# Optimization experiments

Hardware: AMD Instinct MI355X
Metric: run time of the kernel (lower is better)

## Reference

```python
import jax, jax.numpy as jnp
import numpy as np

NUM_HEADS = 16


def setup_inputs() -> dict:
    key = jax.random.key(0)
    ks = jax.random.split(key, 11)
    S, E, F = 4096, 2048, 8192
    s = lambda k, shape, fan_in: jax.random.normal(k, shape, jnp.float32) / np.sqrt(fan_in)
    return {
        "emb": jax.random.normal(ks[0], (S, E), jnp.float32),
        "Wq": s(ks[1], (E, E), E), "bq": jnp.zeros((E,), jnp.float32),
        "Wk": s(ks[2], (E, E), E), "bk": jnp.zeros((E,), jnp.float32),
        "Wv": s(ks[3], (E, E), E), "bv": jnp.zeros((E,), jnp.float32),
        "W1": s(ks[4], (E, F), E), "b1": jnp.zeros((F,), jnp.float32),
        "W2": s(ks[5], (F, E), F), "b2": jnp.zeros((E,), jnp.float32),
    }


def reference(emb, Wq, bq, Wk, bk, Wv, bv, W1, b1, W2, b2):
    S, E = emb.shape
    H = NUM_HEADS
    D = E // H
    # project and split heads -> [H, S, D]
    q = (emb @ Wq + bq).reshape(S, H, D).transpose(1, 0, 2)
    k = (emb @ Wk + bk).reshape(S, H, D).transpose(1, 0, 2)
    v = (emb @ Wv + bv).reshape(S, H, D).transpose(1, 0, 2)
    scale = jnp.asarray(D, emb.dtype) ** 0.5
    scores = jnp.einsum("hsd,htd->hst", q, k) / scale  # [H, S, S]
    # causal mask: additive -1e9 strictly above the diagonal (matches torch.triu(..., 1)*-1e9)
    mask = jnp.triu(jnp.full((S, S), -1e9, dtype=scores.dtype), k=1)
    probs = jax.nn.softmax(scores + mask, axis=-1)
    attn = jnp.einsum("hst,htd->hsd", probs, v)  # [H, S, D]
    attn = attn.transpose(1, 0, 2).reshape(S, E)  # concat heads -> [S, E]
    hidden = jnp.maximum(attn @ W1 + b1, 0.0)
    return hidden @ W2 + b2
```

## Files before the change

### kernel.cpp

```cpp
#include <hip/hip_runtime.h>

typedef __attribute__((ext_vector_type(8))) short bf16x8;
typedef __attribute__((ext_vector_type(4))) float f32x4;
typedef __attribute__((ext_vector_type(8))) unsigned short u16x8;

static constexpr int S = 4096;
static constexpr int E = 2048;
static constexpr int F = 8192;
static constexpr int NH = 16;
static constexpr int DH = 128;

__device__ __forceinline__ unsigned short f2bf(float f) {
  unsigned u = __builtin_bit_cast(unsigned, f);
  u += 0x7FFFu + ((u >> 16) & 1u);
  return (unsigned short)(u >> 16);
}

__device__ __forceinline__ void async16(const unsigned short* g, unsigned short* l) {
  __builtin_amdgcn_global_load_lds(
      (const __attribute__((address_space(1))) unsigned int*)g,
      (__attribute__((address_space(3))) unsigned int*)l, 16, 0, 0);
}

__global__ __launch_bounds__(256) void cvt_bf16_kernel(const float* __restrict__ src,
                                                       unsigned short* __restrict__ dst) {
  int i = (blockIdx.x * 256 + threadIdx.x) * 4;
  float4 v = *(const float4*)(src + i);
  ushort4 o;
  o.x = f2bf(v.x); o.y = f2bf(v.y); o.z = f2bf(v.z); o.w = f2bf(v.w);
  *(ushort4*)(dst + i) = o;
}

__global__ __launch_bounds__(256) void transpose_cvt(const float* __restrict__ src,
                                                     unsigned short* __restrict__ dst,
                                                     const int Rr, const int Cc) {
  __shared__ float t[32][33];
  const int c0 = blockIdx.x * 32, r0 = blockIdx.y * 32;
  const int tx = threadIdx.x, ty = threadIdx.y;
#pragma unroll
  for (int i = 0; i < 4; ++i) {
    int r = ty + i * 8;
    t[r][tx] = src[(size_t)(r0 + r) * Cc + c0 + tx];
  }
  __syncthreads();
#pragma unroll
  for (int i = 0; i < 4; ++i) {
    int cr = ty + i * 8;
    dst[(size_t)(c0 + cr) * Rr + r0 + tx] = f2bf(t[tx][cr]);
  }
}

enum { EPI_QKV = 0, EPI_RELU = 1, EPI_OUT = 2 };

template <int EPI>
__global__ __launch_bounds__(256) void gemm_bt(
    const unsigned short* __restrict__ A, const unsigned short* __restrict__ B,
    const int K, const int N,
    const float* __restrict__ b0, const float* __restrict__ b1f, const float* __restrict__ b2f,
    unsigned short* __restrict__ o0, unsigned short* __restrict__ o1,
    unsigned short* __restrict__ o2, float* __restrict__ of) {
  __shared__ unsigned short lA[2][128 * 32];
  __shared__ unsigned short lB[2][128 * 32];
  const int tid = threadIdx.x, w = tid >> 6, lane = tid & 63;
  const int lane15 = lane & 15, l4 = lane >> 4;
  const int m0 = blockIdx.y * 128, n0 = blockIdx.x * 128;
  const int wr = w >> 1, wc = w & 1;

  const int u0 = (w * 2 + 0) * 64 + lane;
  const int u1 = (w * 2 + 1) * 64 + lane;
  const unsigned short* gA0 = A + (size_t)(m0 + (u0 >> 2)) * K + (u0 & 3) * 8;
  const unsigned short* gA1 = A + (size_t)(m0 + (u1 >> 2)) * K + (u1 & 3) * 8;
  const unsigned short* gB0 = B + (size_t)(n0 + (u0 >> 2)) * K + (u0 & 3) * 8;
  const unsigned short* gB1 = B + (size_t)(n0 + (u1 >> 2)) * K + (u1 & 3) * 8;
  const int doff0 = (w * 2 + 0) * 512;
  const int doff1 = (w * 2 + 1) * 512;

  f32x4 zero4 = {0.f, 0.f, 0.f, 0.f};
  f32x4 acc[4][4];
#pragma unroll
  for (int i = 0; i < 4; ++i)
#pragma unroll
    for (int j = 0; j < 4; ++j) acc[i][j] = zero4;

  async16(gA0, &lA[0][doff0]);
  async16(gA1, &lA[0][doff1]);
  async16(gB0, &lB[0][doff0]);
  async16(gB1, &lB[0][doff1]);

  for (int ko = 0; ko < K; ko += 32) {
    __syncthreads();
    const int buf = (ko >> 5) & 1;
    if (ko + 32 < K) {
      const int nb = buf ^ 1;
      async16(gA0 + ko + 32, &lA[nb][doff0]);
      async16(gA1 + ko + 32, &lA[nb][doff1]);
      async16(gB0 + ko + 32, &lB[nb][doff0]);
      async16(gB1 + ko + 32, &lB[nb][doff1]);
    }
    bf16x8 av[4], bv[4];
#pragma unroll
    for (int i = 0; i < 4; ++i)
      av[i] = *(const bf16x8*)&lA[buf][(wr * 64 + i * 16 + lane15) * 32 + l4 * 8];
#pragma unroll
    for (int j = 0; j < 4; ++j)
      bv[j] = *(const bf16x8*)&lB[buf][(wc * 64 + j * 16 + lane15) * 32 + l4 * 8];
#pragma unroll
    for (int i = 0; i < 4; ++i)
#pragma unroll
      for (int j = 0; j < 4; ++j)
        acc[i][j] = __builtin_amdgcn_mfma_f32_16x16x32_bf16(av[i], bv[j], acc[i][j], 0, 0, 0);
  }

#pragma unroll
  for (int j = 0; j < 4; ++j) {
    const int n = n0 + wc * 64 + j * 16 + lane15;
    float bias;
    if (EPI == EPI_QKV)
      bias = (n < E) ? b0[n] : ((n < 2 * E) ? b1f[n - E] : b2f[n - 2 * E]);
    else
      bias = b0[n];
#pragma unroll
    for (int i = 0; i < 4; ++i) {
      const int mr = m0 + wr * 64 + i * 16 + l4 * 4;
      f32x4 v = acc[i][j];
#pragma unroll
      for (int r = 0; r < 4; ++r) {
        const float val = v[r] + bias;
        const int m = mr + r;
        if (EPI == EPI_QKV) {
          if (n < E)            o0[(size_t)m * E + n] = f2bf(val);
          else if (n < 2 * E)   o1[(size_t)m * E + (n - E)] = f2bf(val);
          else                  o2[(size_t)(n - 2 * E) * S + m] = f2bf(val);
        } else if (EPI == EPI_RELU) {
          o0[(size_t)m * N + n] = f2bf(fmaxf(val, 0.f));
        } else {
          of[(size_t)m * N + n] = val;
        }
      }
    }
  }
}

__global__ __launch_bounds__(256, 2) void flash_attn(const unsigned short* __restrict__ Qb,
                                                     const unsigned short* __restrict__ Kb,
                                                     const unsigned short* __restrict__ VTb,
                                                     unsigned short* __restrict__ attn) {
  const int x = blockIdx.x;
  const int h = blockIdx.y;
  const int qt = (h < 8) ? (31 - x) : x;
  const int qbase = qt * 128;
  const int tid = threadIdx.x, w = tid >> 6, lane = tid & 63;
  const int lane15 = lane & 15, l4 = lane >> 4;
  const int rowb = qbase + w * 32;

  __shared__ unsigned short lK[2][64 * 128];
  __shared__ unsigned short lV[2][128 * 64];
  __shared__ unsigned short lP[4][16 * 72];

  bf16x8 aq[2][4];
#pragma unroll
  for (int rg = 0; rg < 2; ++rg) {
    const unsigned short* qrow = Qb + (size_t)(rowb + rg * 16 + lane15) * E + h * DH + l4 * 8;
#pragma unroll
    for (int kk = 0; kk < 4; ++kk) aq[rg][kk] = *(const bf16x8*)(qrow + kk * 32);
  }

  f32x4 zero4 = {0.f, 0.f, 0.f, 0.f};
  f32x4 o[2][8];
  float psum[2][4];
#pragma unroll
  for (int rg = 0; rg < 2; ++rg) {
#pragma unroll
    for (int j = 0; j < 8; ++j) o[rg][j] = zero4;
#pragma unroll
    for (int r = 0; r < 4; ++r) psum[rg][r] = 0.f;
  }

  {
#pragma unroll
    for (int i = 0; i < 4; ++i) {
      int c = i * 256 + w * 64 + lane;
      int row = c >> 4, pg = (c & 15) ^ (row & 15);
      async16(Kb + (size_t)row * E + h * DH + pg * 8, &lK[0][(i * 256 + w * 64) * 8]);
    }
#pragma unroll
    for (int i = 0; i < 4; ++i) {
      int c = i * 256 + w * 64 + lane;
      int row = c >> 3, pg = (c & 7) ^ (row & 7);
      async16(VTb + (size_t)(h * DH + row) * S + pg * 8, &lV[0][(i * 256 + w * 64) * 8]);
    }
  }

  const float scale = 0.088388347648318447f;
  const int ktmax = 2 * qt + 1;

  for (int kt = 0; kt <= ktmax; ++kt) {
    __syncthreads();
    if (kt < ktmax) {
      const int kb2 = (kt + 1) * 64;
      const int nb = (kt + 1) & 1;
#pragma unroll
      for (int i = 0; i < 4; ++i) {
        int c = i * 256 + w * 64 + lane;
        int row = c >> 4, pg = (c & 15) ^ (row & 15);
        async16(Kb + (size_t)(kb2 + row) * E + h * DH + pg * 8, &lK[nb][(i * 256 + w * 64) * 8]);
      }
#pragma unroll
      for (int i = 0; i < 4; ++i) {
        int c = i * 256 + w * 64 + lane;
        int row = c >> 3, pg = (c & 7) ^ (row & 7);
        async16(VTb + (size_t)(h * DH + row) * S + kb2 + pg * 8, &lV[nb][(i * 256 + w * 64) * 8]);
      }
    }
    if (kt * 64 > rowb + 31) continue;
    const int buf = kt & 1;

    f32x4 sacc[2][4];
#pragma unroll
    for (int rg = 0; rg < 2; ++rg)
#pragma unroll
      for (int j = 0; j < 4; ++j) sacc[rg][j] = zero4;
#pragma unroll
    for (int kk = 0; kk < 4; ++kk)
#pragma unroll
      for (int j = 0; j < 4; ++j) {
        int pl = (kk * 4 + l4) ^ lane15;
        bf16x8 bk = *(const bf16x8*)&lK[buf][(j * 16 + lane15) * 128 + pl * 8];
        sacc[0][j] = __builtin_amdgcn_mfma_f32_16x16x32_bf16(aq[0][kk], bk, sacc[0][j], 0, 0, 0);
        sacc[1][j] = __builtin_amdgcn_mfma_f32_16x16x32_bf16(aq[1][kk], bk, sacc[1][j], 0, 0, 0);
      }

    const bool diag = (kt * 64 + 63 > rowb);
    bf16x8 ap[2][2];
#pragma unroll
    for (int rg = 0; rg < 2; ++rg) {
      float p[4][4];
      if (diag) {
#pragma unroll
        for (int j = 0; j < 4; ++j) {
          int col = kt * 64 + j * 16 + lane15;
#pragma unroll
          for (int r = 0; r < 4; ++r) {
            int row = rowb + rg * 16 + l4 * 4 + r;
            p[j][r] = (col <= row) ? __expf(sacc[rg][j][r] * scale) : 0.f;
          }
        }
      } else {
#pragma unroll
        for (int j = 0; j < 4; ++j)
#pragma unroll
          for (int r = 0; r < 4; ++r) p[j][r] = __expf(sacc[rg][j][r] * scale);
      }
#pragma unroll
      for (int r = 0; r < 4; ++r) psum[rg][r] += p[0][r] + p[1][r] + p[2][r] + p[3][r];

#pragma unroll
      for (int j = 0; j < 4; ++j)
#pragma unroll
        for (int r = 0; r < 4; ++r)
          lP[w][(l4 * 4 + r) * 72 + j * 16 + lane15] = f2bf(p[j][r]);

#pragma unroll
      for (int ks = 0; ks < 2; ++ks)
        ap[rg][ks] = *(const bf16x8*)&lP[w][lane15 * 72 + ks * 32 + l4 * 8];
    }

#pragma unroll
    for (int ks = 0; ks < 2; ++ks)
#pragma unroll
      for (int j = 0; j < 8; ++j) {
        int pl = (ks * 4 + l4) ^ (lane15 & 7);
        bf16x8 bv = *(const bf16x8*)&lV[buf][(j * 16 + lane15) * 64 + pl * 8];
        o[0][j] = __builtin_amdgcn_mfma_f32_16x16x32_bf16(ap[0][ks], bv, o[0][j], 0, 0, 0);
        o[1][j] = __builtin_amdgcn_mfma_f32_16x16x32_bf16(ap[1][ks], bv, o[1][j], 0, 0, 0);
      }
  }

#pragma unroll
  for (int rg = 0; rg < 2; ++rg) {
    float inv[4];
#pragma unroll
    for (int r = 0; r < 4; ++r) {
      float s = psum[rg][r];
#pragma unroll
      for (int off = 1; off < 16; off <<= 1) s += __shfl_xor(s, off, 16);
      inv[r] = 1.0f / s;
    }
#pragma unroll
    for (int j = 0; j < 8; ++j)
#pragma unroll
      for (int r = 0; r < 4; ++r)
        attn[(size_t)(rowb + rg * 16 + l4 * 4 + r) * E + h * DH + j * 16 + lane15] =
            f2bf(o[rg][j][r] * inv[r]);
  }
}

extern "C" void kernel_launch(void* const* d_in, const int* in_sizes, int n_in,
                              void* d_out, int out_size, void* d_ws, size_t ws_size,
                              hipStream_t stream) {
  (void)in_sizes; (void)n_in; (void)out_size; (void)ws_size;
  const float* emb = (const float*)d_in[0];
  const float* Wq  = (const float*)d_in[1];
  const float* bq  = (const float*)d_in[2];
  const float* Wk  = (const float*)d_in[3];
  const float* bk  = (const float*)d_in[4];
  const float* Wv  = (const float*)d_in[5];
  const float* bv  = (const float*)d_in[6];
  const float* W1  = (const float*)d_in[7];
  const float* b1  = (const float*)d_in[8];
  const float* W2  = (const float*)d_in[9];
  const float* b2  = (const float*)d_in[10];
  float* out = (float*)d_out;

  char* ws = (char*)d_ws;
  const size_t MB = 1024ull * 1024ull;
  unsigned short* embb   = (unsigned short*)(ws);
  unsigned short* attn   = embb;
  char* r1 = ws + 16 * MB;
  unsigned short* WqkvT  = (unsigned short*)(r1);
  unsigned short* Qb     = (unsigned short*)(r1 + 24 * MB);
  unsigned short* Kb     = (unsigned short*)(r1 + 40 * MB);
  unsigned short* VTb    = (unsigned short*)(r1 + 56 * MB);
  unsigned short* hidden = (unsigned short*)(r1);
  unsigned short* W1T    = (unsigned short*)(r1 + 72 * MB);
  unsigned short* W2T    = (unsigned short*)(r1 + 104 * MB);

  dim3 b256(256);
  dim3 tb(32, 8);
  cvt_bf16_kernel<<<dim3((S * E) / 1024), b256, 0, stream>>>(emb, embb);
  transpose_cvt<<<dim3(E / 32, E / 32), tb, 0, stream>>>(Wq, WqkvT, E, E);
  transpose_cvt<<<dim3(E / 32, E / 32), tb, 0, stream>>>(Wk, WqkvT + (size_t)E * E, E, E);
  transpose_cvt<<<dim3(E / 32, E / 32), tb, 0, stream>>>(Wv, WqkvT + 2ull * E * E, E, E);
  transpose_cvt<<<dim3(F / 32, E / 32), tb, 0, stream>>>(W1, W1T, E, F);
  transpose_cvt<<<dim3(E / 32, F / 32), tb, 0, stream>>>(W2, W2T, F, E);

  gemm_bt<EPI_QKV><<<dim3(3 * E / 128, S / 128), b256, 0, stream>>>(
      embb, WqkvT, E, 3 * E, bq, bk, bv, Qb, Kb, VTb, nullptr);
  flash_attn<<<dim3(S / 128, NH), b256, 0, stream>>>(Qb, Kb, VTb, attn);
  gemm_bt<EPI_RELU><<<dim3(F / 128, S / 128), b256, 0, stream>>>(
      attn, W1T, E, F, b1, nullptr, nullptr, hidden, nullptr, nullptr, nullptr);
  gemm_bt<EPI_OUT><<<dim3(E / 128, S / 128), b256, 0, stream>>>(
      hidden, W2T, F, E, b2, nullptr, nullptr, nullptr, nullptr, nullptr, out);
}
```

Measured before the change: 852.3 us.

## Replace GEMM with 256x256-tile 8-wave kernel using swizzled LDS and staged prefetch

Replaces the 128x128, 4-wave, K=32 GEMM with a 256x256-tile, 8-wave, K=64 kernel. It XOR-swizzles the LDS layout to avoid bank conflicts, splits each K-step into four MFMA phases that interleave partial global->LDS prefetches with explicit barriers and waitcnts, and raises MFMA priority with setprio. The aim is more data reuse per load and better overlap of memory traffic with matrix math in all three projection GEMMs. In exchange it uses 128 KB of LDS and many more accumulator registers, which may limit occupancy. The hand-placed waitcnt counts are fragile and could cause correctness problems if they are miscounted.

```diff
diff --git a/kernel.cpp b/kernel.cpp
--- a/kernel.cpp
+++ b/kernel.cpp
@@ -2,7 +2,6 @@
 
 typedef __attribute__((ext_vector_type(8))) short bf16x8;
 typedef __attribute__((ext_vector_type(4))) float f32x4;
-typedef __attribute__((ext_vector_type(8))) unsigned short u16x8;
 
 static constexpr int S = 4096;
 static constexpr int E = 2048;
@@ -21,6 +20,23 @@
       (const __attribute__((address_space(1))) unsigned int*)g,
       (__attribute__((address_space(3))) unsigned int*)l, 16, 0, 0);
 }
+
+#define BARRIER()                                     \
+  do {                                                \
+    asm volatile("s_barrier" ::: "memory");           \
+    __builtin_amdgcn_sched_barrier(0);                \
+  } while (0)
+#define WAIT_LGKM0()                                  \
+  do {                                                \
+    asm volatile("s_waitcnt lgkmcnt(0)" ::: "memory");\
+    __builtin_amdgcn_sched_barrier(0);                \
+  } while (0)
+#define WAIT_VM(n)                                    \
+  do {                                                \
+    __builtin_amdgcn_sched_barrier(0);                \
+    asm volatile("s_waitcnt vmcnt(" #n ")" ::: "memory"); \
+    __builtin_amdgcn_sched_barrier(0);                \
+  } while (0)
 
 __global__ __launch_bounds__(256) void cvt_bf16_kernel(const float* __restrict__ src,
                                                        unsigned short* __restrict__ dst) {
@@ -53,62 +69,158 @@
 enum { EPI_QKV = 0, EPI_RELU = 1, EPI_OUT = 2 };
 
 template <int EPI>
-__global__ __launch_bounds__(256) void gemm_bt(
+__global__ __launch_bounds__(512, 2) void gemm8(
     const unsigned short* __restrict__ A, const unsigned short* __restrict__ B,
     const int K, const int N,
     const float* __restrict__ b0, const float* __restrict__ b1f, const float* __restrict__ b2f,
     unsigned short* __restrict__ o0, unsigned short* __restrict__ o1,
     unsigned short* __restrict__ o2, float* __restrict__ of) {
-  __shared__ unsigned short lA[2][128 * 32];
-  __shared__ unsigned short lB[2][128 * 32];
+  __shared__ unsigned short lA[2][256 * 64];
+  __shared__ unsigned short lB[2][256 * 64];
   const int tid = threadIdx.x, w = tid >> 6, lane = tid & 63;
   const int lane15 = lane & 15, l4 = lane >> 4;
-  const int m0 = blockIdx.y * 128, n0 = blockIdx.x * 128;
-  const int wr = w >> 1, wc = w & 1;
-
-  const int u0 = (w * 2 + 0) * 64 + lane;
-  const int u1 = (w * 2 + 1) * 64 + lane;
-  const unsigned short* gA0 = A + (size_t)(m0 + (u0 >> 2)) * K + (u0 & 3) * 8;
-  const unsigned short* gA1 = A + (size_t)(m0 + (u1 >> 2)) * K + (u1 & 3) * 8;
-  const unsigned short* gB0 = B + (size_t)(n0 + (u0 >> 2)) * K + (u0 & 3) * 8;
-  const unsigned short* gB1 = B + (size_t)(n0 + (u1 >> 2)) * K + (u1 & 3) * 8;
-  const int doff0 = (w * 2 + 0) * 512;
-  const int doff1 = (w * 2 + 1) * 512;
+  const int wr = w >> 2, wc = w & 3;
+  const int m0 = blockIdx.y * 256, n0 = blockIdx.x * 256;
+
+  const int prow = tid >> 3;
+  const int pcc = (tid & 7) ^ (prow & 7);
+  const unsigned short* gA = A + (size_t)(m0 + prow) * K + pcc * 8;
+  const unsigned short* gB = B + (size_t)(n0 + prow) * K + pcc * 8;
+  const size_t rstep = (size_t)64 * K;
+  const int lw = w * 512;
+
+  const int pswz0 = l4 ^ (lane15 & 7);
+  const int pswz1 = (4 + l4) ^ (lane15 & 7);
+  const int arow = (wr * 128 + lane15) * 64;
+  const int brow = (wc * 64 + lane15) * 64;
 
   f32x4 zero4 = {0.f, 0.f, 0.f, 0.f};
-  f32x4 acc[4][4];
-#pragma unroll
-  for (int i = 0; i < 4; ++i)
+  f32x4 acc[8][4];
+#pragma unroll
+  for (int i = 0; i < 8; ++i)
 #pragma unroll
     for (int j = 0; j < 4; ++j) acc[i][j] = zero4;
 
-  async16(gA0, &lA[0][doff0]);
-  async16(gA1, &lA[0][doff1]);
-  async16(gB0, &lB[0][doff0]);
-  async16(gB1, &lB[0][doff1]);
-
-  for (int ko = 0; ko < K; ko += 32) {
-    __syncthreads();
-    const int buf = (ko >> 5) & 1;
-    if (ko + 32 < K) {
-      const int nb = buf ^ 1;
-      async16(gA0 + ko + 32, &lA[nb][doff0]);
-      async16(gA1 + ko + 32, &lA[nb][doff1]);
-      async16(gB0 + ko + 32, &lB[nb][doff0]);
-      async16(gB1 + ko + 32, &lB[nb][doff1]);
-    }
-    bf16x8 av[4], bv[4];
-#pragma unroll
-    for (int i = 0; i < 4; ++i)
-      av[i] = *(const bf16x8*)&lA[buf][(wr * 64 + i * 16 + lane15) * 32 + l4 * 8];
-#pragma unroll
-    for (int j = 0; j < 4; ++j)
-      bv[j] = *(const bf16x8*)&lB[buf][(wc * 64 + j * 16 + lane15) * 32 + l4 * 8];
-#pragma unroll
-    for (int i = 0; i < 4; ++i)
-#pragma unroll
-      for (int j = 0; j < 4; ++j)
-        acc[i][j] = __builtin_amdgcn_mfma_f32_16x16x32_bf16(av[i], bv[j], acc[i][j], 0, 0, 0);
+#pragma unroll
+  for (int r = 0; r < 4; ++r) async16(gB + r * rstep, &lB[0][r * 4096 + lw]);
+#pragma unroll
+  for (int r = 0; r < 4; ++r) async16(gA + r * rstep, &lA[0][r * 4096 + lw]);
+  WAIT_VM(0);
+  BARRIER();
+
+  const int NT = K >> 6;
+  bf16x8 a0[4][2], bb[2][2];
+  for (int t = 0; t < NT; ++t) {
+    const unsigned short* lAb = lA[t & 1];
+    const unsigned short* lBb = lB[t & 1];
+    unsigned short* lAn = lA[(t & 1) ^ 1];
+    unsigned short* lBn = lB[(t & 1) ^ 1];
+    const size_t ko = (size_t)(t + 1) * 64;
+    const bool nxt = (t + 1 < NT);
+
+#pragma unroll
+    for (int mi = 0; mi < 4; ++mi) {
+      a0[mi][0] = *(const bf16x8*)&lAb[arow + mi * 1024 + pswz0 * 8];
+      a0[mi][1] = *(const bf16x8*)&lAb[arow + mi * 1024 + pswz1 * 8];
+    }
+#pragma unroll
+    for (int nj = 0; nj < 2; ++nj) {
+      bb[nj][0] = *(const bf16x8*)&lBb[brow + nj * 1024 + pswz0 * 8];
+      bb[nj][1] = *(const bf16x8*)&lBb[brow + nj * 1024 + pswz1 * 8];
+    }
+    if (nxt) {
+      async16(gB + 0 * rstep + ko, &lBn[0 * 4096 + lw]);
+      async16(gB + 1 * rstep + ko, &lBn[1 * 4096 + lw]);
+    }
+    BARRIER();
+    WAIT_LGKM0();
+    __builtin_amdgcn_s_setprio(1);
+#pragma unroll
+    for (int mi = 0; mi < 4; ++mi)
+#pragma unroll
+      for (int nj = 0; nj < 2; ++nj)
+#pragma unroll
+        for (int kk = 0; kk < 2; ++kk)
+          acc[mi][nj] = __builtin_amdgcn_mfma_f32_16x16x32_bf16(a0[mi][kk], bb[nj][kk], acc[mi][nj], 0, 0, 0);
+    __builtin_amdgcn_s_setprio(0);
+    BARRIER();
+
+#pragma unroll
+    for (int nj = 0; nj < 2; ++nj) {
+      bb[nj][0] = *(const bf16x8*)&lBb[brow + 2048 + nj * 1024 + pswz0 * 8];
+      bb[nj][1] = *(const bf16x8*)&lBb[brow + 2048 + nj * 1024 + pswz1 * 8];
+    }
+    if (nxt) {
+      async16(gB + 2 * rstep + ko, &lBn[2 * 4096 + lw]);
+      async16(gB + 3 * rstep + ko, &lBn[3 * 4096 + lw]);
+    }
+    BARRIER();
+    WAIT_LGKM0();
+    __builtin_amdgcn_s_setprio(1);
+#pragma unroll
+    for (int mi = 0; mi < 4; ++mi)
+#pragma unroll
+      for (int nj = 0; nj < 2; ++nj)
+#pragma unroll
+        for (int kk = 0; kk < 2; ++kk)
+          acc[mi][2 + nj] = __builtin_amdgcn_mfma_f32_16x16x32_bf16(a0[mi][kk], bb[nj][kk], acc[mi][2 + nj], 0, 0, 0);
+    __builtin_amdgcn_s_setprio(0);
+    if (nxt)
+      WAIT_VM(4);
+    else
+      WAIT_VM(0);
+    BARRIER();
+
+#pragma unroll
+    for (int mi = 0; mi < 4; ++mi) {
+      a0[mi][0] = *(const bf16x8*)&lAb[arow + 4096 + mi * 1024 + pswz0 * 8];
+      a0[mi][1] = *(const bf16x8*)&lAb[arow + 4096 + mi * 1024 + pswz1 * 8];
+    }
+#pragma unroll
+    for (int nj = 0; nj < 2; ++nj) {
+      bb[nj][0] = *(const bf16x8*)&lBb[brow + nj * 1024 + pswz0 * 8];
+      bb[nj][1] = *(const bf16x8*)&lBb[brow + nj * 1024 + pswz1 * 8];
+    }
+    if (nxt) {
+      async16(gA + 0 * rstep + ko, &lAn[0 * 4096 + lw]);
+      async16(gA + 2 * rstep + ko, &lAn[2 * 4096 + lw]);
+    }
+    BARRIER();
+    WAIT_LGKM0();
+    __builtin_amdgcn_s_setprio(1);
+#pragma unroll
+    for (int mi = 0; mi < 4; ++mi)
+#pragma unroll
+      for (int nj = 0; nj < 2; ++nj)
+#pragma unroll
+        for (int kk = 0; kk < 2; ++kk)
+          acc[4 + mi][nj] = __builtin_amdgcn_mfma_f32_16x16x32_bf16(a0[mi][kk], bb[nj][kk], acc[4 + mi][nj], 0, 0, 0);
+    __builtin_amdgcn_s_setprio(0);
+    BARRIER();
+
+#pragma unroll
+    for (int nj = 0; nj < 2; ++nj) {
+      bb[nj][0] = *(const bf16x8*)&lBb[brow + 2048 + nj * 1024 + pswz0 * 8];
+      bb[nj][1] = *(const bf16x8*)&lBb[brow + 2048 + nj * 1024 + pswz1 * 8];
+    }
+    if (nxt) {
+      async16(gA + 1 * rstep + ko, &lAn[1 * 4096 + lw]);
+      async16(gA + 3 * rstep + ko, &lAn[3 * 4096 + lw]);
+    }
+    BARRIER();
+    WAIT_LGKM0();
+    __builtin_amdgcn_s_setprio(1);
+#pragma unroll
+    for (int mi = 0; mi < 4; ++mi)
+#pragma unroll
+      for (int nj = 0; nj < 2; ++nj)
+#pragma unroll
+        for (int kk = 0; kk < 2; ++kk)
+          acc[4 + mi][2 + nj] = __builtin_amdgcn_mfma_f32_16x16x32_bf16(a0[mi][kk], bb[nj][kk], acc[4 + mi][2 + nj], 0, 0, 0);
+    __builtin_amdgcn_s_setprio(0);
+    if (nxt)
+      WAIT_VM(2);
+    BARRIER();
   }
 
 #pragma unroll
@@ -120,8 +232,8 @@
     else
       bias = b0[n];
 #pragma unroll
-    for (int i = 0; i < 4; ++i) {
-      const int mr = m0 + wr * 64 + i * 16 + l4 * 4;
+    for (int i = 0; i < 8; ++i) {
+      const int mr = m0 + wr * 128 + i * 16 + l4 * 4;
       f32x4 v = acc[i][j];
 #pragma unroll
       for (int r = 0; r < 4; ++r) {
@@ -326,6 +438,7 @@
   unsigned short* W2T    = (unsigned short*)(r1 + 104 * MB);
 
   dim3 b256(256);
+  dim3 b512(512);
   dim3 tb(32, 8);
   cvt_bf16_kernel<<<dim3((S * E) / 1024), b256, 0, stream>>>(emb, embb);
   transpose_cvt<<<dim3(E / 32, E / 32), tb, 0, stream>>>(Wq, WqkvT, E, E);
@@ -334,11 +447,11 @@
   transpose_cvt<<<dim3(F / 32, E / 32), tb, 0, stream>>>(W1, W1T, E, F);
   transpose_cvt<<<dim3(E / 32, F / 32), tb, 0, stream>>>(W2, W2T, F, E);
 
-  gemm_bt<EPI_QKV><<<dim3(3 * E / 128, S / 128), b256, 0, stream>>>(
+  gemm8<EPI_QKV><<<dim3(3 * E / 256, S / 256), b512, 0, stream>>>(
       embb, WqkvT, E, 3 * E, bq, bk, bv, Qb, Kb, VTb, nullptr);
   flash_attn<<<dim3(S / 128, NH), b256, 0, stream>>>(Qb, Kb, VTb, attn);
-  gemm_bt<EPI_RELU><<<dim3(F / 128, S / 128), b256, 0, stream>>>(
+  gemm8<EPI_RELU><<<dim3(F / 256, S / 256), b512, 0, stream>>>(
       attn, W1T, E, F, b1, nullptr, nullptr, hidden, nullptr, nullptr, nullptr);
-  gemm_bt<EPI_OUT><<<dim3(E / 128, S / 128), b256, 0, stream>>>(
+  gemm8<EPI_OUT><<<dim3(E / 256, S / 256), b512, 0, stream>>>(
       hidden, W2T, F, E, b2, nullptr, nullptr, nullptr, nullptr, nullptr, out);
 }
```

Result: slower. 906.2 us (+6.3%).
